# Performance work log

Hardware: AMD Instinct MI355X
Metric: run time of the kernel (lower is better)

The kernel has to match this reference:

```python
import jax, jax.numpy as jnp
import numpy as np

PAA_SIZE = 64  # init_kwargs paa_size
GAF_TYPE = 'GADF'  # init_kwargs GAF_type


def setup_inputs() -> dict:
    key = jax.random.key(0)
    x = jax.random.uniform(key, (256, 4096, 32), dtype=jnp.float32)
    return {"x": x}


def reference(x):
    # x: [B, T, C]
    B, T, C = x.shape
    # --- rescale: per-sample, per-channel min-max over time axis -> [0, 1]
    x_min = jnp.min(x, axis=1, keepdims=True)
    x_max = jnp.max(x, axis=1, keepdims=True)
    r = (x - x_min) / (x_max - x_min)            # [B, T, C]
    # --- PAA: strided mean over bins of length size = T // paa_size
    size = T // PAA_SIZE
    p = r[:, : PAA_SIZE * size].reshape(B, PAA_SIZE, size, C).sum(axis=2) / size  # [B, P, C]
    # --- GAF construction
    y = jnp.sqrt(1.0 - p * p)                    # [B, P, C]
    if GAF_TYPE == 'GASF':
        # out[b,i,j,c] = x_i x_j - y_i y_j (symmetric)
        out = jnp.einsum('bic,bjc->bijc', p, p) - jnp.einsum('bic,bjc->bijc', y, y)
    else:  # 'GADF'
        # original: -transpose(y x^T - x y^T) => out[b,i,j,c] = y_i x_j - x_i y_j
        out = jnp.einsum('bic,bjc->bijc', y, p) - jnp.einsum('bic,bjc->bijc', p, y)
    return out  # [B, paa_size, paa_size, C]
```

## Files before the change

kernel.cpp:

```cpp
#include <hip/hip_runtime.h>
#include <math.h>

#define BB   256
#define TT   4096
#define CC   32
#define PP   64
#define PSTR 36

__device__ __forceinline__ float4 f4min(float4 a, float4 b) {
    return make_float4(fminf(a.x,b.x), fminf(a.y,b.y), fminf(a.z,b.z), fminf(a.w,b.w));
}
__device__ __forceinline__ float4 f4max(float4 a, float4 b) {
    return make_float4(fmaxf(a.x,b.x), fmaxf(a.y,b.y), fmaxf(a.z,b.z), fmaxf(a.w,b.w));
}
__device__ __forceinline__ void f4add(float4& a, float4 v) {
    a.x += v.x; a.y += v.y; a.z += v.z; a.w += v.w;
}
__device__ __forceinline__ float4 shflxor4(float4 v, int m) {
    return make_float4(__shfl_xor(v.x, m), __shfl_xor(v.y, m),
                       __shfl_xor(v.z, m), __shfl_xor(v.w, m));
}

__global__ __launch_bounds__(256) void gaf_kernel(const float* __restrict__ x,
                                                  float* __restrict__ out) {
    __shared__ float sp[PP * PSTR];
    __shared__ float sy[PP * PSTR];
    __shared__ float redmin[4 * CC];
    __shared__ float redmax[4 * CC];

    const int tid  = threadIdx.x;
    const int cg   = tid & 7;
    const int rb   = tid >> 3;
    const int wave = tid >> 6;
    const int lane = tid & 63;
    const int b    = blockIdx.x;

    const float4* x4 = (const float4*)x + (size_t)b * (TT * CC / 4) + rb * 1024 + cg;

    const float FBIG = 3.402823466e+38f;
    float4 mn = make_float4(FBIG, FBIG, FBIG, FBIG);
    float4 mx = make_float4(-FBIG, -FBIG, -FBIG, -FBIG);
    float4 a0 = make_float4(0.f, 0.f, 0.f, 0.f);
    float4 a1 = make_float4(0.f, 0.f, 0.f, 0.f);

    #pragma unroll 8
    for (int k = 0; k < 64; ++k) {
        float4 v = x4[k * 8];
        mn = f4min(mn, v); mx = f4max(mx, v); f4add(a0, v);
    }
    #pragma unroll 8
    for (int k = 64; k < 128; ++k) {
        float4 v = x4[k * 8];
        mn = f4min(mn, v); mx = f4max(mx, v); f4add(a1, v);
    }

    #pragma unroll
    for (int m = 8; m <= 32; m <<= 1) {
        mn = f4min(mn, shflxor4(mn, m));
        mx = f4max(mx, shflxor4(mx, m));
    }
    if (lane < 8) {
        *(float4*)&redmin[wave * CC + cg * 4] = mn;
        *(float4*)&redmax[wave * CC + cg * 4] = mx;
    }
    __syncthreads();

    float4 gmn = *(const float4*)&redmin[0 * CC + cg * 4];
    float4 gmx = *(const float4*)&redmax[0 * CC + cg * 4];
    #pragma unroll
    for (int w = 1; w < 4; ++w) {
        gmn = f4min(gmn, *(const float4*)&redmin[w * CC + cg * 4]);
        gmx = f4max(gmx, *(const float4*)&redmax[w * CC + cg * 4]);
    }

    float4 inv;
    inv.x = 1.0f / (gmx.x - gmn.x);
    inv.y = 1.0f / (gmx.y - gmn.y);
    inv.z = 1.0f / (gmx.z - gmn.z);
    inv.w = 1.0f / (gmx.w - gmn.w);

    float4 p0, p1, y0, y1;
    const float s64 = 1.0f / 64.0f;
    p0.x = (a0.x * s64 - gmn.x) * inv.x;  p0.y = (a0.y * s64 - gmn.y) * inv.y;
    p0.z = (a0.z * s64 - gmn.z) * inv.z;  p0.w = (a0.w * s64 - gmn.w) * inv.w;
    p1.x = (a1.x * s64 - gmn.x) * inv.x;  p1.y = (a1.y * s64 - gmn.y) * inv.y;
    p1.z = (a1.z * s64 - gmn.z) * inv.z;  p1.w = (a1.w * s64 - gmn.w) * inv.w;
    y0.x = sqrtf(fmaxf(1.f - p0.x * p0.x, 0.f));  y0.y = sqrtf(fmaxf(1.f - p0.y * p0.y, 0.f));
    y0.z = sqrtf(fmaxf(1.f - p0.z * p0.z, 0.f));  y0.w = sqrtf(fmaxf(1.f - p0.w * p0.w, 0.f));
    y1.x = sqrtf(fmaxf(1.f - p1.x * p1.x, 0.f));  y1.y = sqrtf(fmaxf(1.f - p1.y * p1.y, 0.f));
    y1.z = sqrtf(fmaxf(1.f - p1.z * p1.z, 0.f));  y1.w = sqrtf(fmaxf(1.f - p1.w * p1.w, 0.f));

    *(float4*)&sp[(2 * rb)     * PSTR + cg * 4] = p0;
    *(float4*)&sp[(2 * rb + 1) * PSTR + cg * 4] = p1;
    *(float4*)&sy[(2 * rb)     * PSTR + cg * 4] = y0;
    *(float4*)&sy[(2 * rb + 1) * PSTR + cg * 4] = y1;
    __syncthreads();

    const int j1 = rb, j2 = rb + 32;
    const float4 pj1 = *(const float4*)&sp[j1 * PSTR + cg * 4];
    const float4 yj1 = *(const float4*)&sy[j1 * PSTR + cg * 4];
    const float4 pj2 = *(const float4*)&sp[j2 * PSTR + cg * 4];
    const float4 yj2 = *(const float4*)&sy[j2 * PSTR + cg * 4];

    float4* o4 = (float4*)out + (size_t)b * (PP * PP * CC / 4);

    #pragma unroll 4
    for (int i = 0; i < PP; ++i) {
        const float4 pi = *(const float4*)&sp[i * PSTR + cg * 4];
        const float4 yi = *(const float4*)&sy[i * PSTR + cg * 4];
        float4 r1, r2;
        r1.x = yi.x * pj1.x - pi.x * yj1.x;  r1.y = yi.y * pj1.y - pi.y * yj1.y;
        r1.z = yi.z * pj1.z - pi.z * yj1.z;  r1.w = yi.w * pj1.w - pi.w * yj1.w;
        r2.x = yi.x * pj2.x - pi.x * yj2.x;  r2.y = yi.y * pj2.y - pi.y * yj2.y;
        r2.z = yi.z * pj2.z - pi.z * yj2.z;  r2.w = yi.w * pj2.w - pi.w * yj2.w;
        o4[i * 512 + j1 * 8 + cg] = r1;
        o4[i * 512 + j2 * 8 + cg] = r2;
    }
}

extern "C" void kernel_launch(void* const* d_in, const int* in_sizes, int n_in,
                              void* d_out, int out_size, void* d_ws, size_t ws_size,
                              hipStream_t stream) {
    const float* x = (const float*)d_in[0];
    float* out = (float*)d_out;
    gaf_kernel<<<BB, 256, 0, stream>>>(x, out);
}
```

Baseline: 233.0 us.

## Use 1024 threads per block, splitting each PAA bin across two row groups

Measured after the change: 237.8 us. +2.0%, slower.

```diff
diff --git a/kernel.cpp b/kernel.cpp
--- a/kernel.cpp
+++ b/kernel.cpp
@@ -21,12 +21,12 @@
                        __shfl_xor(v.z, m), __shfl_xor(v.w, m));
 }
 
-__global__ __launch_bounds__(256) void gaf_kernel(const float* __restrict__ x,
-                                                  float* __restrict__ out) {
+__global__ __launch_bounds__(1024) void gaf_kernel(const float* __restrict__ x,
+                                                   float* __restrict__ out) {
     __shared__ float sp[PP * PSTR];
     __shared__ float sy[PP * PSTR];
-    __shared__ float redmin[4 * CC];
-    __shared__ float redmax[4 * CC];
+    __shared__ float redmin[16 * CC];
+    __shared__ float redmax[16 * CC];
 
     const int tid  = threadIdx.x;
     const int cg   = tid & 7;
@@ -35,24 +35,21 @@
     const int lane = tid & 63;
     const int b    = blockIdx.x;
 
-    const float4* x4 = (const float4*)x + (size_t)b * (TT * CC / 4) + rb * 1024 + cg;
+    const float4* x4 = (const float4*)x + (size_t)b * (TT * CC / 4) + rb * 256 + cg;
 
     const float FBIG = 3.402823466e+38f;
     float4 mn = make_float4(FBIG, FBIG, FBIG, FBIG);
     float4 mx = make_float4(-FBIG, -FBIG, -FBIG, -FBIG);
-    float4 a0 = make_float4(0.f, 0.f, 0.f, 0.f);
-    float4 a1 = make_float4(0.f, 0.f, 0.f, 0.f);
+    float4 acc = make_float4(0.f, 0.f, 0.f, 0.f);
 
     #pragma unroll 8
-    for (int k = 0; k < 64; ++k) {
+    for (int k = 0; k < 32; ++k) {
         float4 v = x4[k * 8];
-        mn = f4min(mn, v); mx = f4max(mx, v); f4add(a0, v);
+        mn = f4min(mn, v); mx = f4max(mx, v); f4add(acc, v);
     }
-    #pragma unroll 8
-    for (int k = 64; k < 128; ++k) {
-        float4 v = x4[k * 8];
-        mn = f4min(mn, v); mx = f4max(mx, v); f4add(a1, v);
-    }
+
+    float4 seg = acc;
+    f4add(seg, shflxor4(acc, 8));
 
     #pragma unroll
     for (int m = 8; m <= 32; m <<= 1) {
@@ -68,53 +65,45 @@
     float4 gmn = *(const float4*)&redmin[0 * CC + cg * 4];
     float4 gmx = *(const float4*)&redmax[0 * CC + cg * 4];
     #pragma unroll
-    for (int w = 1; w < 4; ++w) {
+    for (int w = 1; w < 16; ++w) {
         gmn = f4min(gmn, *(const float4*)&redmin[w * CC + cg * 4]);
         gmx = f4max(gmx, *(const float4*)&redmax[w * CC + cg * 4]);
     }
 
-    float4 inv;
-    inv.x = 1.0f / (gmx.x - gmn.x);
-    inv.y = 1.0f / (gmx.y - gmn.y);
-    inv.z = 1.0f / (gmx.z - gmn.z);
-    inv.w = 1.0f / (gmx.w - gmn.w);
-
-    float4 p0, p1, y0, y1;
-    const float s64 = 1.0f / 64.0f;
-    p0.x = (a0.x * s64 - gmn.x) * inv.x;  p0.y = (a0.y * s64 - gmn.y) * inv.y;
-    p0.z = (a0.z * s64 - gmn.z) * inv.z;  p0.w = (a0.w * s64 - gmn.w) * inv.w;
-    p1.x = (a1.x * s64 - gmn.x) * inv.x;  p1.y = (a1.y * s64 - gmn.y) * inv.y;
-    p1.z = (a1.z * s64 - gmn.z) * inv.z;  p1.w = (a1.w * s64 - gmn.w) * inv.w;
-    y0.x = sqrtf(fmaxf(1.f - p0.x * p0.x, 0.f));  y0.y = sqrtf(fmaxf(1.f - p0.y * p0.y, 0.f));
-    y0.z = sqrtf(fmaxf(1.f - p0.z * p0.z, 0.f));  y0.w = sqrtf(fmaxf(1.f - p0.w * p0.w, 0.f));
-    y1.x = sqrtf(fmaxf(1.f - p1.x * p1.x, 0.f));  y1.y = sqrtf(fmaxf(1.f - p1.y * p1.y, 0.f));
-    y1.z = sqrtf(fmaxf(1.f - p1.z * p1.z, 0.f));  y1.w = sqrtf(fmaxf(1.f - p1.w * p1.w, 0.f));
-
-    *(float4*)&sp[(2 * rb)     * PSTR + cg * 4] = p0;
-    *(float4*)&sp[(2 * rb + 1) * PSTR + cg * 4] = p1;
-    *(float4*)&sy[(2 * rb)     * PSTR + cg * 4] = y0;
-    *(float4*)&sy[(2 * rb + 1) * PSTR + cg * 4] = y1;
+    if ((rb & 1) == 0) {
+        const int s = rb >> 1;
+        float4 inv;
+        inv.x = 1.0f / (gmx.x - gmn.x);
+        inv.y = 1.0f / (gmx.y - gmn.y);
+        inv.z = 1.0f / (gmx.z - gmn.z);
+        inv.w = 1.0f / (gmx.w - gmn.w);
+        const float s64 = 1.0f / 64.0f;
+        float4 p, y;
+        p.x = (seg.x * s64 - gmn.x) * inv.x;  p.y = (seg.y * s64 - gmn.y) * inv.y;
+        p.z = (seg.z * s64 - gmn.z) * inv.z;  p.w = (seg.w * s64 - gmn.w) * inv.w;
+        y.x = sqrtf(fmaxf(1.f - p.x * p.x, 0.f));  y.y = sqrtf(fmaxf(1.f - p.y * p.y, 0.f));
+        y.z = sqrtf(fmaxf(1.f - p.z * p.z, 0.f));  y.w = sqrtf(fmaxf(1.f - p.w * p.w, 0.f));
+        *(float4*)&sp[s * PSTR + cg * 4] = p;
+        *(float4*)&sy[s * PSTR + cg * 4] = y;
+    }
     __syncthreads();
 
-    const int j1 = rb, j2 = rb + 32;
-    const float4 pj1 = *(const float4*)&sp[j1 * PSTR + cg * 4];
-    const float4 yj1 = *(const float4*)&sy[j1 * PSTR + cg * 4];
-    const float4 pj2 = *(const float4*)&sp[j2 * PSTR + cg * 4];
-    const float4 yj2 = *(const float4*)&sy[j2 * PSTR + cg * 4];
+    const int j  = (tid >> 3) & 63;
+    const int ih = tid >> 9;
+    const float4 pj = *(const float4*)&sp[j * PSTR + cg * 4];
+    const float4 yj = *(const float4*)&sy[j * PSTR + cg * 4];
 
     float4* o4 = (float4*)out + (size_t)b * (PP * PP * CC / 4);
 
-    #pragma unroll 4
-    for (int i = 0; i < PP; ++i) {
+    #pragma unroll 8
+    for (int ii = 0; ii < 32; ++ii) {
+        const int i = ih * 32 + ii;
         const float4 pi = *(const float4*)&sp[i * PSTR + cg * 4];
         const float4 yi = *(const float4*)&sy[i * PSTR + cg * 4];
-        float4 r1, r2;
-        r1.x = yi.x * pj1.x - pi.x * yj1.x;  r1.y = yi.y * pj1.y - pi.y * yj1.y;
-        r1.z = yi.z * pj1.z - pi.z * yj1.z;  r1.w = yi.w * pj1.w - pi.w * yj1.w;
-        r2.x = yi.x * pj2.x - pi.x * yj2.x;  r2.y = yi.y * pj2.y - pi.y * yj2.y;
-        r2.z = yi.z * pj2.z - pi.z * yj2.z;  r2.w = yi.w * pj2.w - pi.w * yj2.w;
-        o4[i * 512 + j1 * 8 + cg] = r1;
-        o4[i * 512 + j2 * 8 + cg] = r2;
+        float4 r;
+        r.x = yi.x * pj.x - pi.x * yj.x;  r.y = yi.y * pj.y - pi.y * yj.y;
+        r.z = yi.z * pj.z - pi.z * yj.z;  r.w = yi.w * pj.w - pi.w * yj.w;
+        o4[i * 512 + j * 8 + cg] = r;
     }
 }
 
@@ -123,5 +112,5 @@
                               hipStream_t stream) {
     const float* x = (const float*)d_in[0];
     float* out = (float*)d_out;
-    gaf_kernel<<<BB, 256, 0, stream>>>(x, out);
+    gaf_kernel<<<BB, 1024, 0, stream>>>(x, out);
 }
```
